# Performance work log

Measured on AMD Instinct MI355X. Metric: run time of the kernel, lower is better.

## Reference

```python
import jax, jax.numpy as jnp
import numpy as np

N = 100000

def gat_layer(x, src, dst, W, a_s, a_d, b, H, C, concat):
    # x: [N, F_in]; messages flow src -> dst, softmax grouped by dst (PyG GATConv)
    h = (x @ W).reshape(N, H, C)                       # [N,H,C]
    al_s = jnp.sum(h * a_s, axis=-1)                   # [N,H]
    al_d = jnp.sum(h * a_d, axis=-1)                   # [N,H]
    e = jax.nn.leaky_relu(al_s[src] + al_d[dst], 0.2)  # [E,H]
    m = jax.ops.segment_max(e, dst, num_segments=N)    # [N,H] per-dst max
    ex = jnp.exp(e - m[dst])
    s = jax.ops.segment_sum(ex, dst, num_segments=N)
    alpha = ex / (s[dst] + 1e-16)                      # [E,H]
    msg = h[src] * alpha[:, :, None]                   # [E,H,C]
    out = jax.ops.segment_sum(msg, dst, num_segments=N)  # [N,H,C]
    out = out.reshape(N, H * C) if concat else out.mean(axis=1)
    return out + b

def setup_inputs() -> dict:
    key = jax.random.key(0)
    ks = jax.random.split(key, 32)
    d = {}
    d['x'] = jax.random.normal(ks[0], (N, 128), dtype=jnp.float32)
    d['edge_index'] = jax.random.randint(ks[1], (2, 1600000), 0, N, dtype=jnp.int32)
    dims = [(128, 8, 8), (64, 8, 8), (64, 8, 8), (64, 8, 8), (64, 8, 40)]
    for i, (fin, H, C) in enumerate(dims, start=1):
        d[f'W{i}'] = jax.random.normal(ks[4 * i], (fin, H * C), dtype=jnp.float32) * 0.1
        d[f'as{i}'] = jax.random.normal(ks[4 * i + 1], (H, C), dtype=jnp.float32) * 0.1
        d[f'ad{i}'] = jax.random.normal(ks[4 * i + 2], (H, C), dtype=jnp.float32) * 0.1
        d[f'b{i}'] = jnp.zeros((H * C if i < 5 else C,), dtype=jnp.float32)
    return d

def reference(x, edge_index, W1, as1, ad1, b1, W2, as2, ad2, b2, W3, as3, ad3, b3, W4, as4, ad4, b4, W5, as5, ad5, b5):
    # add self-loops (PyG GATConv default add_self_loops=True)
    loop = jnp.arange(N, dtype=edge_index.dtype)
    src = jnp.concatenate([edge_index[0], loop])
    dst = jnp.concatenate([edge_index[1], loop])
    h = gat_layer(x, src, dst, W1, as1, ad1, b1, 8, 8, True)
    h = jax.nn.leaky_relu(h, 0.2)  # dropout is identity in eval mode
    h = gat_layer(h, src, dst, W2, as2, ad2, b2, 8, 8, True)
    h = jax.nn.leaky_relu(h, 0.2)
    h = gat_layer(h, src, dst, W3, as3, ad3, b3, 8, 8, True)
    h = jax.nn.leaky_relu(h, 0.2)
    h = gat_layer(h, src, dst, W4, as4, ad4, b4, 8, 8, True)
    h = jax.nn.leaky_relu(h, 0.2)
    h = gat_layer(h, src, dst, W5, as5, ad5, b5, 8, 40, False)
    return jax.nn.log_softmax(h, axis=1)
```

## Files before the change

### kernel.cpp

```cpp
#include <hip/hip_runtime.h>
#include <cstddef>
#include <cstdint>

static __device__ __forceinline__ float leaky(float x){ return x >= 0.f ? x : 0.2f*x; }
static __device__ __forceinline__ float bfl(unsigned short v){ return __uint_as_float(((unsigned)v)<<16); }
static __device__ __forceinline__ float blo(unsigned u){ return __uint_as_float(u<<16); }
static __device__ __forceinline__ float bhi(unsigned u){ return __uint_as_float(u & 0xffff0000u); }
static __device__ __forceinline__ unsigned bf16r(float f){
  unsigned u = __float_as_uint(f);
  return (u + 0x7fffu + ((u>>16)&1u)) >> 16;
}
static __device__ __forceinline__ unsigned pk(float lo, float hi){
  return bf16r(lo) | (bf16r(hi)<<16);
}

__global__ __launch_bounds__(256) void rs_hist1(const int* __restrict__ edst, int E, int N,
                                                int* __restrict__ hist, int NBLK, int Etot){
  __shared__ int lh[512];
  int t = threadIdx.x, b = blockIdx.x;
  lh[t] = 0; lh[t+256] = 0;
  __syncthreads();
  int base = b*8192;
  for (int i = 0; i < 32; i++){
    int e = base + t + i*256;
    if (e < Etot){
      int d = (e < E) ? edst[e] : (e - E);
      atomicAdd(&lh[d>>8], 1);
    }
  }
  __syncthreads();
  hist[(size_t)t*NBLK + b] = lh[t];
  hist[(size_t)(t+256)*NBLK + b] = lh[t+256];
}
__global__ __launch_bounds__(256) void s_bsum(const int* __restrict__ a, int* __restrict__ bsum, int L){
  __shared__ int sm[256];
  int t = threadIdx.x; int i = blockIdx.x*256 + t;
  sm[t] = (i < L) ? a[i] : 0;
  __syncthreads();
  #pragma unroll
  for (int o=128;o;o>>=1){ if (t<o) sm[t]+=sm[t+o]; __syncthreads(); }
  if (t==0) bsum[blockIdx.x] = sm[0];
}
__global__ __launch_bounds__(512) void k_bscan(const int* __restrict__ bsum, int* __restrict__ boff, int NB){
  __shared__ int sm[512];
  int t = threadIdx.x;
  int v = (t < NB) ? bsum[t] : 0;
  sm[t] = v; __syncthreads();
  for (int o=1;o<512;o<<=1){
    int u = (t>=o) ? sm[t-o] : 0;
    __syncthreads();
    sm[t] += u;
    __syncthreads();
  }
  if (t < NB) boff[t] = sm[t] - v;
  if (t == NB-1) boff[NB] = sm[t];
}
__global__ __launch_bounds__(256) void s_apply(const int* __restrict__ a, const int* __restrict__ boff,
                                               int* __restrict__ out, int L){
  __shared__ int sm[256];
  int t = threadIdx.x, b = blockIdx.x;
  int i = b*256 + t;
  int v = (i < L) ? a[i] : 0;
  sm[t] = v; __syncthreads();
  for (int o=1;o<256;o<<=1){
    int u = (t>=o) ? sm[t-o] : 0;
    __syncthreads();
    sm[t] += u;
    __syncthreads();
  }
  if (i < L) out[i] = boff[b] + sm[t] - v;
}
__global__ __launch_bounds__(256) void rs_scatter1(const int* __restrict__ esrc, const int* __restrict__ edst,
                                                   int E, int N, const int* __restrict__ hist2, int NBLK,
                                                   int2* __restrict__ bufA, int Etot){
  __shared__ int gb[512];
  __shared__ int lcnt[512];
  int t = threadIdx.x, b = blockIdx.x;
  gb[t]     = hist2[(size_t)t*NBLK + b];
  gb[t+256] = hist2[(size_t)(t+256)*NBLK + b];
  lcnt[t] = 0; lcnt[t+256] = 0;
  __syncthreads();
  int base = b*8192;
  for (int i = 0; i < 32; i++){
    int e = base + t + i*256;
    if (e < Etot){
      int s, d;
      if (e < E){ s = esrc[e]; d = edst[e]; }
      else { s = e - E; d = s; }
      int bin = d >> 8;
      int r = atomicAdd(&lcnt[bin], 1);
      bufA[gb[bin] + r] = make_int2(s, d);
    }
  }
}
__global__ __launch_bounds__(256) void rs_lvl2(const int2* __restrict__ bufA, const int* __restrict__ hist2,
                                               int NBLK, int* __restrict__ srcs, int* __restrict__ off,
                                               int N, int Etot){
  __shared__ int cnt[256];
  __shared__ int basev[256];
  int t = threadIdx.x, g = blockIdx.x;
  int beg = hist2[(size_t)g*NBLK];
  int end = (g < 511) ? hist2[(size_t)(g+1)*NBLK] : Etot;
  cnt[t] = 0;
  __syncthreads();
  for (int j = beg + t; j < end; j += 256)
    atomicAdd(&cnt[bufA[j].y & 255], 1);
  __syncthreads();
  int v = cnt[t];
  for (int o=1;o<256;o<<=1){
    int u = (t>=o) ? cnt[t-o] : 0;
    __syncthreads();
    cnt[t] += u;
    __syncthreads();
  }
  basev[t] = cnt[t] - v;
  __syncthreads();
  cnt[t] = 0;
  __syncthreads();
  for (int j = beg + t; j < end; j += 256){
    int2 p = bufA[j];
    int lb = p.y & 255;
    int r = atomicAdd(&cnt[lb], 1);
    srcs[beg + basev[lb] + r] = p.x;
  }
  int node = g*256 + t;
  if (node < N) off[node] = beg + basev[t];
  if (g == 0 && t == 0) off[N] = Etot;
}

template<int K, int M, bool OB>
__global__ __launch_bounds__(256) void k_gemm(
    const float* __restrict__ A, const float* __restrict__ W, int ldw, int col0,
    void* __restrict__ out, int N)
{
  constexpr int KT = 64;
  constexpr int TX = M/4;
  __shared__ float As[64][KT+1];
  __shared__ alignas(16) float Ws[KT][M];
  int t = threadIdx.x;
  int base = blockIdx.x*64;
  int tx = t % TX, ty = t / TX;
  bool act = ty < 16;
  int n0 = ty*4, m0 = tx*4;
  float acc[4][4] = {};
  for (int kt=0; kt<K; kt+=KT){
    for (int i=t; i<64*(KT/4); i+=256){
      int n  = i >> 4;
      int kq = i & 15;
      float4 v = make_float4(0.f,0.f,0.f,0.f);
      int gn = base + n;
      if (gn < N) v = *(const float4*)(A + (size_t)gn*K + kt + kq*4);
      As[n][kq*4+0]=v.x; As[n][kq*4+1]=v.y; As[n][kq*4+2]=v.z; As[n][kq*4+3]=v.w;
    }
    for (int i=t; i<KT*(M/4); i+=256){
      int k = i/(M/4), mq = i%(M/4);
      *(float4*)&Ws[k][mq*4] = *(const float4*)(W + (size_t)(kt+k)*ldw + col0 + mq*4);
    }
    __syncthreads();
    if (act){
      #pragma unroll 8
      for (int k=0;k<KT;k++){
        float4 w = *(const float4*)&Ws[k][m0];
        float av0 = As[n0+0][k], av1 = As[n0+1][k], av2 = As[n0+2][k], av3 = As[n0+3][k];
        acc[0][0]=fmaf(av0,w.x,acc[0][0]); acc[0][1]=fmaf(av0,w.y,acc[0][1]);
        acc[0][2]=fmaf(av0,w.z,acc[0][2]); acc[0][3]=fmaf(av0,w.w,acc[0][3]);
        acc[1][0]=fmaf(av1,w.x,acc[1][0]); acc[1][1]=fmaf(av1,w.y,acc[1][1]);
        acc[1][2]=fmaf(av1,w.z,acc[1][2]); acc[1][3]=fmaf(av1,w.w,acc[1][3]);
        acc[2][0]=fmaf(av2,w.x,acc[2][0]); acc[2][1]=fmaf(av2,w.y,acc[2][1]);
        acc[2][2]=fmaf(av2,w.z,acc[2][2]); acc[2][3]=fmaf(av2,w.w,acc[2][3]);
        acc[3][0]=fmaf(av3,w.x,acc[3][0]); acc[3][1]=fmaf(av3,w.y,acc[3][1]);
        acc[3][2]=fmaf(av3,w.z,acc[3][2]); acc[3][3]=fmaf(av3,w.w,acc[3][3]);
      }
    }
    __syncthreads();
  }
  if (act){
    #pragma unroll
    for (int i=0;i<4;i++){
      int gn = base + n0 + i;
      if (gn < N){
        if (OB){
          unsigned p0 = pk(acc[i][0], acc[i][1]);
          unsigned p1 = pk(acc[i][2], acc[i][3]);
          *(uint2*)((unsigned short*)out + (size_t)gn*M + m0) = make_uint2(p0, p1);
        } else {
          float4 v = make_float4(acc[i][0],acc[i][1],acc[i][2],acc[i][3]);
          *(float4*)((float*)out + (size_t)gn*M + m0) = v;
        }
      }
    }
  }
}

__global__ __launch_bounds__(320) void k_gemm5(
    const unsigned short* __restrict__ z16, const float* __restrict__ Wf,
    float* __restrict__ out5, int base, int cnt)
{
  __shared__ float As[64][65];
  __shared__ alignas(16) float Ws[64][40];
  int t = threadIdx.x;
  int rb = blockIdx.x*64;
  int tx = t % 10, ty = t / 10;
  int n0 = ty*2, m0 = tx*4;
  float acc[2][4] = {};
  for (int kt = 0; kt < 512; kt += 64){
    for (int i = t; i < 512; i += 320){
      int n = i >> 3, kq = i & 7;
      uint4 q = make_uint4(0,0,0,0);
      int ln = rb + n;
      if (ln < cnt) q = *(const uint4*)(z16 + (size_t)ln*512 + kt + kq*8);
      float* ap = &As[n][kq*8];
      ap[0]=blo(q.x); ap[1]=bhi(q.x); ap[2]=blo(q.y); ap[3]=bhi(q.y);
      ap[4]=blo(q.z); ap[5]=bhi(q.z); ap[6]=blo(q.w); ap[7]=bhi(q.w);
    }
    for (int i = t; i < 640; i += 320){
      int k = i / 10, mq = i % 10;
      *(float4*)&Ws[k][mq*4] = *(const float4*)(Wf + (size_t)(kt+k)*40 + mq*4);
    }
    __syncthreads();
    #pragma unroll 8
    for (int k=0;k<64;k++){
      float4 w = *(const float4*)&Ws[k][m0];
      float a0 = As[n0][k], a1 = As[n0+1][k];
      acc[0][0]=fmaf(a0,w.x,acc[0][0]); acc[0][1]=fmaf(a0,w.y,acc[0][1]);
      acc[0][2]=fmaf(a0,w.z,acc[0][2]); acc[0][3]=fmaf(a0,w.w,acc[0][3]);
      acc[1][0]=fmaf(a1,w.x,acc[1][0]); acc[1][1]=fmaf(a1,w.y,acc[1][1]);
      acc[1][2]=fmaf(a1,w.z,acc[1][2]); acc[1][3]=fmaf(a1,w.w,acc[1][3]);
    }
    __syncthreads();
  }
  #pragma unroll
  for (int r=0;r<2;r++){
    int ln = rb + n0 + r;
    if (ln < cnt){
      *(float4*)(out5 + (size_t)(base+ln)*40 + m0) =
        make_float4(acc[r][0],acc[r][1],acc[r][2],acc[r][3]);
    }
  }
}

__global__ void k_al(const unsigned short* __restrict__ h16, const float* __restrict__ a_s,
                     const float* __restrict__ a_d, unsigned short* __restrict__ al_s16,
                     float* __restrict__ al_d, int total )
{
  int idx = blockIdx.x*256 + threadIdx.x;
  if (idx >= total) return;
  int hd = idx & 7;
  uint4 q = *(const uint4*)(h16 + (size_t)idx*8);
  const float4* sp = (const float4*)(a_s + hd*8);
  const float4* dp = (const float4*)(a_d + hd*8);
  float4 s0 = sp[0], s1 = sp[1], d0 = dp[0], d1 = dp[1];
  float f0=blo(q.x), f1=bhi(q.x), f2=blo(q.y), f3=bhi(q.y);
  float f4=blo(q.z), f5=bhi(q.z), f6=blo(q.w), f7=bhi(q.w);
  float s = f0*s0.x + f1*s0.y + f2*s0.z + f3*s0.w
          + f4*s1.x + f5*s1.y + f6*s1.z + f7*s1.w;
  float d = f0*d0.x + f1*d0.y + f2*d0.z + f3*d0.w
          + f4*d1.x + f5*d1.y + f6*d1.z + f7*d1.w;
  al_s16[idx] = (unsigned short)bf16r(s);
  al_d[idx] = d;
}

template<bool OB>
__global__ __launch_bounds__(256) void k_agg64(
    const unsigned short* __restrict__ h16, const unsigned short* __restrict__ al16,
    const float* __restrict__ al_d, const int* __restrict__ off,
    const int* __restrict__ srcs, const float* __restrict__ bias,
    void* __restrict__ outf, int N, int apply_act)
{
  int t = threadIdx.x;
  int grp = t >> 3;
  int sub = t & 7;
  int node = blockIdx.x*32 + grp;
  if (node >= N) return;
  int beg = off[node], end = off[node+1];
  float ald = al_d[(size_t)node*8 + sub];
  float s = 0.f;
  float acc[8] = {0.f,0.f,0.f,0.f,0.f,0.f,0.f,0.f};
  int j = beg;
  for (; j+3 < end; j += 4){
    int s0 = srcs[j], s1 = srcs[j+1], s2 = srcs[j+2], s3 = srcs[j+3];
    float e0 = leaky(bfl(al16[(size_t)s0*8 + sub]) + ald);
    float e1 = leaky(bfl(al16[(size_t)s1*8 + sub]) + ald);
    float e2 = leaky(bfl(al16[(size_t)s2*8 + sub]) + ald);
    float e3 = leaky(bfl(al16[(size_t)s3*8 + sub]) + ald);
    float a0 = __expf(e0), a1 = __expf(e1), a2 = __expf(e2), a3 = __expf(e3);
    uint4 q0 = *(const uint4*)(h16 + (size_t)s0*64 + sub*8);
    uint4 q1 = *(const uint4*)(h16 + (size_t)s1*64 + sub*8);
    uint4 q2 = *(const uint4*)(h16 + (size_t)s2*64 + sub*8);
    uint4 q3 = *(const uint4*)(h16 + (size_t)s3*64 + sub*8);
    s += a0 + a1 + a2 + a3;
    acc[0]=fmaf(a0,blo(q0.x),acc[0]); acc[1]=fmaf(a0,bhi(q0.x),acc[1]);
    acc[2]=fmaf(a0,blo(q0.y),acc[2]); acc[3]=fmaf(a0,bhi(q0.y),acc[3]);
    acc[4]=fmaf(a0,blo(q0.z),acc[4]); acc[5]=fmaf(a0,bhi(q0.z),acc[5]);
    acc[6]=fmaf(a0,blo(q0.w),acc[6]); acc[7]=fmaf(a0,bhi(q0.w),acc[7]);
    acc[0]=fmaf(a1,blo(q1.x),acc[0]); acc[1]=fmaf(a1,bhi(q1.x),acc[1]);
    acc[2]=fmaf(a1,blo(q1.y),acc[2]); acc[3]=fmaf(a1,bhi(q1.y),acc[3]);
    acc[4]=fmaf(a1,blo(q1.z),acc[4]); acc[5]=fmaf(a1,bhi(q1.z),acc[5]);
    acc[6]=fmaf(a1,blo(q1.w),acc[6]); acc[7]=fmaf(a1,bhi(q1.w),acc[7]);
    acc[0]=fmaf(a2,blo(q2.x),acc[0]); acc[1]=fmaf(a2,bhi(q2.x),acc[1]);
    acc[2]=fmaf(a2,blo(q2.y),acc[2]); acc[3]=fmaf(a2,bhi(q2.y),acc[3]);
    acc[4]=fmaf(a2,blo(q2.z),acc[4]); acc[5]=fmaf(a2,bhi(q2.z),acc[5]);
    acc[6]=fmaf(a2,blo(q2.w),acc[6]); acc[7]=fmaf(a2,bhi(q2.w),acc[7]);
    acc[0]=fmaf(a3,blo(q3.x),acc[0]); acc[1]=fmaf(a3,bhi(q3.x),acc[1]);
    acc[2]=fmaf(a3,blo(q3.y),acc[2]); acc[3]=fmaf(a3,bhi(q3.y),acc[3]);
    acc[4]=fmaf(a3,blo(q3.z),acc[4]); acc[5]=fmaf(a3,bhi(q3.z),acc[5]);
    acc[6]=fmaf(a3,blo(q3.w),acc[6]); acc[7]=fmaf(a3,bhi(q3.w),acc[7]);
  }
  for (; j < end; ++j){
    int s0 = srcs[j];
    float e0 = leaky(bfl(al16[(size_t)s0*8 + sub]) + ald);
    float a0 = __expf(e0);
    uint4 q0 = *(const uint4*)(h16 + (size_t)s0*64 + sub*8);
    s += a0;
    acc[0]=fmaf(a0,blo(q0.x),acc[0]); acc[1]=fmaf(a0,bhi(q0.x),acc[1]);
    acc[2]=fmaf(a0,blo(q0.y),acc[2]); acc[3]=fmaf(a0,bhi(q0.y),acc[3]);
    acc[4]=fmaf(a0,blo(q0.z),acc[4]); acc[5]=fmaf(a0,bhi(q0.z),acc[5]);
    acc[6]=fmaf(a0,blo(q0.w),acc[6]); acc[7]=fmaf(a0,bhi(q0.w),acc[7]);
  }
  float inv = 1.f/(s + 1e-16f);
  const float4* bp = (const float4*)(bias + sub*8);
  float4 b0 = bp[0], b1 = bp[1];
  float r0 = acc[0]*inv + b0.x, r1 = acc[1]*inv + b0.y;
  float r2 = acc[2]*inv + b0.z, r3 = acc[3]*inv + b0.w;
  float r4 = acc[4]*inv + b1.x, r5 = acc[5]*inv + b1.y;
  float r6 = acc[6]*inv + b1.z, r7 = acc[7]*inv + b1.w;
  if (apply_act){
    r0=leaky(r0); r1=leaky(r1); r2=leaky(r2); r3=leaky(r3);
    r4=leaky(r4); r5=leaky(r5); r6=leaky(r6); r7=leaky(r7);
  }
  if (OB){
    uint4 o;
    o.x = pk(r0,r1); o.y = pk(r2,r3); o.z = pk(r4,r5); o.w = pk(r6,r7);
    *(uint4*)((unsigned short*)outf + (size_t)node*64 + sub*8) = o;
  } else {
    float* op = (float*)outf + (size_t)node*64 + sub*8;
    *(float4*)op = make_float4(r0,r1,r2,r3);
    *(float4*)(op+4) = make_float4(r4,r5,r6,r7);
  }
}

__global__ __launch_bounds__(512) void k_ws(const float* __restrict__ W5,
                                            const float* __restrict__ as5,
                                            const float* __restrict__ ad5,
                                            float* __restrict__ ws, float* __restrict__ wd){
  int t = threadIdx.x;
  int h = t >> 6, k = t & 63;
  float s = 0.f, d = 0.f;
  #pragma unroll 8
  for (int c=0;c<40;c++){
    float w = W5[(size_t)k*320 + h*40 + c];
    s = fmaf(w, as5[h*40+c], s);
    d = fmaf(w, ad5[h*40+c], d);
  }
  ws[h*64+k] = s; wd[h*64+k] = d;
}
__global__ void k_wf(const float* __restrict__ W5, float* __restrict__ Wf){
  int i = blockIdx.x*256 + threadIdx.x;
  if (i >= 512*40) return;
  int row = i / 40, c = i - row*40;
  int h = row >> 6, k = row & 63;
  Wf[i] = W5[(size_t)k*320 + h*40 + c];
}
__global__ void k_al5b(const unsigned short* __restrict__ f16, const float* __restrict__ ws,
                       const float* __restrict__ wd, unsigned short* __restrict__ al_s16,
                       float* __restrict__ al_d, int total )
{
  int idx = blockIdx.x*256 + threadIdx.x;
  if (idx >= total) return;
  int n = idx >> 3, h = idx & 7;
  const uint4* fp = (const uint4*)(f16 + (size_t)n*64);
  const float4* ap = (const float4*)(ws + h*64);
  const float4* bp = (const float4*)(wd + h*64);
  float s = 0.f, d = 0.f;
  #pragma unroll
  for (int q=0;q<8;q++){
    uint4 f = fp[q];
    float4 a0 = ap[q*2], a1 = ap[q*2+1];
    float4 b0 = bp[q*2], b1 = bp[q*2+1];
    float f0=blo(f.x), f1=bhi(f.x), f2=blo(f.y), f3=bhi(f.y);
    float f4=blo(f.z), f5=bhi(f.z), f6=blo(f.w), f7=bhi(f.w);
    s += f0*a0.x + f1*a0.y + f2*a0.z + f3*a0.w + f4*a1.x + f5*a1.y + f6*a1.z + f7*a1.w;
    d += f0*b0.x + f1*b0.y + f2*b0.z + f3*b0.w + f4*b1.x + f5*b1.y + f6*b1.z + f7*b1.w;
  }
  al_s16[idx] = (unsigned short)bf16r(s);
  al_d[idx] = d;
}

__global__ __launch_bounds__(256) void k_agg5z(
    const unsigned short* __restrict__ f16, const unsigned short* __restrict__ al16,
    const float* __restrict__ al_d, const int* __restrict__ off,
    const int* __restrict__ srcs, unsigned short* __restrict__ z16, int base, int cnt)
{
  int t = threadIdx.x;
  int w = t >> 6;
  int ln = blockIdx.x*4 + w;
  if (ln >= cnt) return;
  int node = base + ln;
  int tl = t & 63;
  int hd = tl & 7;
  int cb = tl >> 3;
  int beg = off[node], end = off[node+1];
  float ald = al_d[(size_t)node*8 + hd];
  int lanebase = hd*4;
  int cbo = cb*8;
  float s = 0.f;
  float acc[8] = {0.f,0.f,0.f,0.f,0.f,0.f,0.f,0.f};
  for (int jb = beg; jb < end; jb += 8){
    int j = jb + cb;
    float atil = 0.f; int si = 0;
    if (j < end){
      si = srcs[j];
      atil = __expf(leaky(bfl(al16[(size_t)si*8 + hd]) + ald));
    }
    s += atil;
    #pragma unroll 8
    for (int e = 0; e < 8; e++){
      if (jb + e >= end) break;
      float ae = __uint_as_float(__builtin_amdgcn_ds_bpermute(lanebase + e*32, __float_as_uint(atil)));
      int sie = __builtin_amdgcn_readlane(si, e*8);
      uint4 q = *(const uint4*)(f16 + (size_t)sie*64 + cbo);
      acc[0]=fmaf(ae,blo(q.x),acc[0]); acc[1]=fmaf(ae,bhi(q.x),acc[1]);
      acc[2]=fmaf(ae,blo(q.y),acc[2]); acc[3]=fmaf(ae,bhi(q.y),acc[3]);
      acc[4]=fmaf(ae,blo(q.z),acc[4]); acc[5]=fmaf(ae,bhi(q.z),acc[5]);
      acc[6]=fmaf(ae,blo(q.w),acc[6]); acc[7]=fmaf(ae,bhi(q.w),acc[7]);
    }
  }
  s += __shfl_xor(s, 8, 64);
  s += __shfl_xor(s, 16, 64);
  s += __shfl_xor(s, 32, 64);
  float inv = 1.f/(s + 1e-16f);
  uint4 o;
  o.x = pk(acc[0]*inv, acc[1]*inv);
  o.y = pk(acc[2]*inv, acc[3]*inv);
  o.z = pk(acc[4]*inv, acc[5]*inv);
  o.w = pk(acc[6]*inv, acc[7]*inv);
  *(uint4*)(z16 + (size_t)ln*512 + hd*64 + cbo) = o;
}

__global__ __launch_bounds__(256) void k_final(
    const float* __restrict__ acc, const float* __restrict__ b5,
    float* __restrict__ out, int N)
{
  int t = threadIdx.x;
  int node = blockIdx.x*4 + (t >> 6);
  if (node >= N) return;
  int tl = t & 63;
  float v = (tl < 40) ? acc[(size_t)node*40 + tl]*0.125f + b5[tl] : -1e30f;
  float m = v;
  #pragma unroll
  for (int o=32;o;o>>=1) m = fmaxf(m, __shfl_xor(m, o, 64));
  float ex = (tl < 40) ? __expf(v - m) : 0.f;
  float s = ex;
  #pragma unroll
  for (int o=32;o;o>>=1) s += __shfl_xor(s, o, 64);
  if (tl < 40) out[(size_t)node*40 + tl] = (v - m) - __logf(s);
}

extern "C" void kernel_launch(void* const* d_in, const int* in_sizes, int n_in,
                              void* d_out, int out_size, void* d_ws, size_t ws_size,
                              hipStream_t stream) {
  const float* x  = (const float*)d_in[0];
  const int*   ei = (const int*)d_in[1];
  const int N = in_sizes[0] / 128;
  const int E = in_sizes[1] / 2;
  const int* esrc = ei;
  const int* edst = ei + E;
  const float* W1 = (const float*)d_in[2];
  const float* as1= (const float*)d_in[3];
  const float* ad1= (const float*)d_in[4];
  const float* b1 = (const float*)d_in[5];
  const float* W2 = (const float*)d_in[6];
  const float* as2= (const float*)d_in[7];
  const float* ad2= (const float*)d_in[8];
  const float* b2 = (const float*)d_in[9];
  const float* W3 = (const float*)d_in[10];
  const float* as3= (const float*)d_in[11];
  const float* ad3= (const float*)d_in[12];
  const float* b3 = (const float*)d_in[13];
  const float* W4 = (const float*)d_in[14];
  const float* as4= (const float*)d_in[15];
  const float* ad4= (const float*)d_in[16];
  const float* b4 = (const float*)d_in[17];
  const float* W5 = (const float*)d_in[18];
  const float* as5= (const float*)d_in[19];
  const float* ad5= (const float*)d_in[20];
  const float* b5 = (const float*)d_in[21];

  char* p = (char*)d_ws;
  auto alloc = [&](size_t bytes)->void*{
    uintptr_t u = (uintptr_t)p;
    u = (u + 255) & ~(uintptr_t)255;
    void* r = (void*)u;
    p = (char*)u + bytes;
    return r;
  };
  const int Etot = E + N;
  const int NBLK = (Etot + 8191)/8192;
  const int L    = 512*NBLK;
  const int NB2  = (L + 255)/256;
  const int NG   = (N + 255)/256;

  int* off    = (int*)alloc((size_t)(N+1)*4);
  int* srcs   = (int*)alloc((size_t)Etot*4);
  int* hist   = (int*)alloc((size_t)L*4);
  int* hist2  = (int*)alloc((size_t)L*4);
  int* hb     = (int*)alloc((size_t)(NB2+1)*4);
  unsigned short* al_s16 = (unsigned short*)alloc((size_t)N*8*2);
  float* al_d = (float*)alloc((size_t)N*8*4);
  unsigned short* h16  = (unsigned short*)alloc((size_t)N*64*2);
  unsigned short* fB16 = (unsigned short*)alloc((size_t)N*64*2);
  float* featA= (float*)alloc((size_t)N*64*4);
  float* featB= (float*)alloc((size_t)N*64*4);
  float* wsb  = (float*)alloc((size_t)8*64*4);
  float* wdb  = (float*)alloc((size_t)8*64*4);
  float* Wf   = (float*)alloc((size_t)512*40*4);
  float* out5 = (float*)alloc((size_t)N*40*4);
  unsigned short* zbuf = (unsigned short*)featA;
  int2* bufA  = (int2*)featA;

  int gT = (N+63)/64, gA = (N+3)/4;
  int gA64 = (N+31)/32;
  int gAl = (N*8+255)/256;

  rs_hist1  <<<NBLK,256,0,stream>>>(edst, E, N, hist, NBLK, Etot);
  s_bsum    <<<NB2,256,0,stream>>>(hist, hb, L);
  k_bscan   <<<1,512,0,stream>>>(hb, hb, NB2);
  s_apply   <<<NB2,256,0,stream>>>(hist, hb, hist2, L);
  rs_scatter1<<<NBLK,256,0,stream>>>(esrc, edst, E, N, hist2, NBLK, bufA, Etot);
  rs_lvl2   <<<NG,256,0,stream>>>(bufA, hist2, NBLK, srcs, off, N, Etot);

  k_gemm<128,64,true><<<gT,256,0,stream>>>(x, W1, 64, 0, h16, N);
  k_al<<<gAl,256,0,stream>>>(h16, as1, ad1, al_s16, al_d, N*8);
  k_agg64<false><<<gA64,256,0,stream>>>(h16, al_s16, al_d, off, srcs, b1, featA, N, 1);

  k_gemm<64,64,true><<<gT,256,0,stream>>>(featA, W2, 64, 0, h16, N);
  k_al<<<gAl,256,0,stream>>>(h16, as2, ad2, al_s16, al_d, N*8);
  k_agg64<false><<<gA64,256,0,stream>>>(h16, al_s16, al_d, off, srcs, b2, featB, N, 1);

  k_gemm<64,64,true><<<gT,256,0,stream>>>(featB, W3, 64, 0, h16, N);
  k_al<<<gAl,256,0,stream>>>(h16, as3, ad3, al_s16, al_d, N*8);
  k_agg64<false><<<gA64,256,0,stream>>>(h16, al_s16, al_d, off, srcs, b3, featA, N, 1);

  k_gemm<64,64,true><<<gT,256,0,stream>>>(featA, W4, 64, 0, h16, N);
  k_al<<<gAl,256,0,stream>>>(h16, as4, ad4, al_s16, al_d, N*8);
  k_agg64<true><<<gA64,256,0,stream>>>(h16, al_s16, al_d, off, srcs, b4, fB16, N, 1);

  k_ws  <<<1,512,0,stream>>>(W5, as5, ad5, wsb, wdb);
  k_wf  <<<(512*40+255)/256,256,0,stream>>>(W5, Wf);
  k_al5b<<<gAl,256,0,stream>>>(fB16, wsb, wdb, al_s16, al_d, N*8);
  const int CH = 50000;
  for (int base = 0; base < N; base += CH){
    int cnt = (N - base < CH) ? (N - base) : CH;
    k_agg5z<<<(cnt+3)/4,256,0,stream>>>(fB16, al_s16, al_d, off, srcs, zbuf, base, cnt);
    k_gemm5<<<(cnt+63)/64,320,0,stream>>>(zbuf, Wf, out5, base, cnt);
  }

  k_final<<<gA,256,0,stream>>>(out5, b5, (float*)d_out, N);
}
```

Measured before the change: 653.3 us.

## Store intermediate features in bf16, pack sort keys, prefetch edges in final aggregation

Intermediate layer activations are written as bf16 and the GEMM gains a bf16-input load path, halving feature traffic between layers. The radix-sort scratch packs the source id and local destination bits into one 32-bit word instead of an int2. The final aggregation kernel software-prefetches the next edge batch's source and attention weight. The chunk size is halved so the scratch buffer can alias the now-dead projection buffer; this relies on N fitting in 17 bits and on buffer adjacency, and adds bf16 rounding on intermediate activations.

Result: slower. 714.7 us (+9.4%).

```diff
diff --git a/kernel.cpp b/kernel.cpp
--- a/kernel.cpp
+++ b/kernel.cpp
@@ -72,7 +72,7 @@
 }
 __global__ __launch_bounds__(256) void rs_scatter1(const int* __restrict__ esrc, const int* __restrict__ edst,
                                                    int E, int N, const int* __restrict__ hist2, int NBLK,
-                                                   int2* __restrict__ bufA, int Etot){
+                                                   int* __restrict__ bufA, int Etot){
   __shared__ int gb[512];
   __shared__ int lcnt[512];
   int t = threadIdx.x, b = blockIdx.x;
@@ -89,11 +89,11 @@
       else { s = e - E; d = s; }
       int bin = d >> 8;
       int r = atomicAdd(&lcnt[bin], 1);
-      bufA[gb[bin] + r] = make_int2(s, d);
-    }
-  }
-}
-__global__ __launch_bounds__(256) void rs_lvl2(const int2* __restrict__ bufA, const int* __restrict__ hist2,
+      bufA[gb[bin] + r] = s | ((d & 255) << 17);
+    }
+  }
+}
+__global__ __launch_bounds__(256) void rs_lvl2(const int* __restrict__ bufA, const int* __restrict__ hist2,
                                                int NBLK, int* __restrict__ srcs, int* __restrict__ off,
                                                int N, int Etot){
   __shared__ int cnt[256];
@@ -104,7 +104,7 @@
   cnt[t] = 0;
   __syncthreads();
   for (int j = beg + t; j < end; j += 256)
-    atomicAdd(&cnt[bufA[j].y & 255], 1);
+    atomicAdd(&cnt[(bufA[j] >> 17) & 255], 1);
   __syncthreads();
   int v = cnt[t];
   for (int o=1;o<256;o<<=1){
@@ -118,19 +118,19 @@
   cnt[t] = 0;
   __syncthreads();
   for (int j = beg + t; j < end; j += 256){
-    int2 p = bufA[j];
-    int lb = p.y & 255;
+    int u = bufA[j];
+    int lb = (u >> 17) & 255;
     int r = atomicAdd(&cnt[lb], 1);
-    srcs[beg + basev[lb] + r] = p.x;
+    srcs[beg + basev[lb] + r] = u & 0x1FFFF;
   }
   int node = g*256 + t;
   if (node < N) off[node] = beg + basev[t];
   if (g == 0 && t == 0) off[N] = Etot;
 }
 
-template<int K, int M, bool OB>
+template<int K, int M, bool IB, bool OB>
 __global__ __launch_bounds__(256) void k_gemm(
-    const float* __restrict__ A, const float* __restrict__ W, int ldw, int col0,
+    const void* __restrict__ Ain, const float* __restrict__ W, int ldw, int col0,
     void* __restrict__ out, int N)
 {
   constexpr int KT = 64;
@@ -144,13 +144,27 @@
   int n0 = ty*4, m0 = tx*4;
   float acc[4][4] = {};
   for (int kt=0; kt<K; kt+=KT){
-    for (int i=t; i<64*(KT/4); i+=256){
-      int n  = i >> 4;
-      int kq = i & 15;
-      float4 v = make_float4(0.f,0.f,0.f,0.f);
-      int gn = base + n;
-      if (gn < N) v = *(const float4*)(A + (size_t)gn*K + kt + kq*4);
-      As[n][kq*4+0]=v.x; As[n][kq*4+1]=v.y; As[n][kq*4+2]=v.z; As[n][kq*4+3]=v.w;
+    if (IB){
+      const unsigned short* A16 = (const unsigned short*)Ain;
+      for (int i=t; i<64*8; i+=256){
+        int n = i >> 3, kq = i & 7;
+        uint4 q = make_uint4(0,0,0,0);
+        int gn = base + n;
+        if (gn < N) q = *(const uint4*)(A16 + (size_t)gn*K + kt + kq*8);
+        float* ap = &As[n][kq*8];
+        ap[0]=blo(q.x); ap[1]=bhi(q.x); ap[2]=blo(q.y); ap[3]=bhi(q.y);
+        ap[4]=blo(q.z); ap[5]=bhi(q.z); ap[6]=blo(q.w); ap[7]=bhi(q.w);
+      }
+    } else {
+      const float* A = (const float*)Ain;
+      for (int i=t; i<64*16; i+=256){
+        int n  = i >> 4;
+        int kq = i & 15;
+        float4 v = make_float4(0.f,0.f,0.f,0.f);
+        int gn = base + n;
+        if (gn < N) v = *(const float4*)(A + (size_t)gn*K + kt + kq*4);
+        As[n][kq*4+0]=v.x; As[n][kq*4+1]=v.y; As[n][kq*4+2]=v.z; As[n][kq*4+3]=v.w;
+      }
     }
     for (int i=t; i<KT*(M/4); i+=256){
       int k = i/(M/4), mq = i%(M/4);
@@ -260,12 +274,11 @@
   al_d[idx] = d;
 }
 
-template<bool OB>
 __global__ __launch_bounds__(256) void k_agg64(
     const unsigned short* __restrict__ h16, const unsigned short* __restrict__ al16,
     const float* __restrict__ al_d, const int* __restrict__ off,
     const int* __restrict__ srcs, const float* __restrict__ bias,
-    void* __restrict__ outf, int N, int apply_act)
+    unsigned short* __restrict__ outf, int N, int apply_act)
 {
   int t = threadIdx.x;
   int grp = t >> 3;
@@ -328,15 +341,9 @@
     r0=leaky(r0); r1=leaky(r1); r2=leaky(r2); r3=leaky(r3);
     r4=leaky(r4); r5=leaky(r5); r6=leaky(r6); r7=leaky(r7);
   }
-  if (OB){
-    uint4 o;
-    o.x = pk(r0,r1); o.y = pk(r2,r3); o.z = pk(r4,r5); o.w = pk(r6,r7);
-    *(uint4*)((unsigned short*)outf + (size_t)node*64 + sub*8) = o;
-  } else {
-    float* op = (float*)outf + (size_t)node*64 + sub*8;
-    *(float4*)op = make_float4(r0,r1,r2,r3);
-    *(float4*)(op+4) = make_float4(r4,r5,r6,r7);
-  }
+  uint4 o;
+  o.x = pk(r0,r1); o.y = pk(r2,r3); o.z = pk(r4,r5); o.w = pk(r6,r7);
+  *(uint4*)(outf + (size_t)node*64 + sub*8) = o;
 }
 
 __global__ __launch_bounds__(512) void k_ws(const float* __restrict__ W5,
@@ -405,17 +412,24 @@
   int cbo = cb*8;
   float s = 0.f;
   float acc[8] = {0.f,0.f,0.f,0.f,0.f,0.f,0.f,0.f};
-  for (int jb = beg; jb < end; jb += 8){
+  int jb = beg;
+  float atil = 0.f; int si = 0;
+  {
     int j = jb + cb;
-    float atil = 0.f; int si = 0;
-    if (j < end){
-      si = srcs[j];
-      atil = __expf(leaky(bfl(al16[(size_t)si*8 + hd]) + ald));
+    if (j < end){ si = srcs[j]; atil = __expf(leaky(bfl(al16[(size_t)si*8 + hd]) + ald)); }
+  }
+  while (jb < end){
+    int jb2 = jb + 8;
+    float atil2 = 0.f; int si2 = 0;
+    {
+      int j2 = jb2 + cb;
+      if (j2 < end){ si2 = srcs[j2]; atil2 = __expf(leaky(bfl(al16[(size_t)si2*8 + hd]) + ald)); }
     }
     s += atil;
+    int nfull = end - jb; if (nfull > 8) nfull = 8;
     #pragma unroll 8
     for (int e = 0; e < 8; e++){
-      if (jb + e >= end) break;
+      if (e >= nfull) break;
       float ae = __uint_as_float(__builtin_amdgcn_ds_bpermute(lanebase + e*32, __float_as_uint(atil)));
       int sie = __builtin_amdgcn_readlane(si, e*8);
       uint4 q = *(const uint4*)(f16 + (size_t)sie*64 + cbo);
@@ -424,6 +438,7 @@
       acc[4]=fmaf(ae,blo(q.z),acc[4]); acc[5]=fmaf(ae,bhi(q.z),acc[5]);
       acc[6]=fmaf(ae,blo(q.w),acc[6]); acc[7]=fmaf(ae,bhi(q.w),acc[7]);
     }
+    atil = atil2; si = si2; jb = jb2;
   }
   s += __shfl_xor(s, 8, 64);
   s += __shfl_xor(s, 16, 64);
@@ -508,15 +523,14 @@
   unsigned short* al_s16 = (unsigned short*)alloc((size_t)N*8*2);
   float* al_d = (float*)alloc((size_t)N*8*4);
   unsigned short* h16  = (unsigned short*)alloc((size_t)N*64*2);
+  unsigned short* fA16 = (unsigned short*)alloc((size_t)N*64*2);
   unsigned short* fB16 = (unsigned short*)alloc((size_t)N*64*2);
-  float* featA= (float*)alloc((size_t)N*64*4);
-  float* featB= (float*)alloc((size_t)N*64*4);
   float* wsb  = (float*)alloc((size_t)8*64*4);
   float* wdb  = (float*)alloc((size_t)8*64*4);
   float* Wf   = (float*)alloc((size_t)512*40*4);
   float* out5 = (float*)alloc((size_t)N*40*4);
-  unsigned short* zbuf = (unsigned short*)featA;
-  int2* bufA  = (int2*)featA;
+  unsigned short* zbuf = h16;
+  int* bufA   = (int*)h16;
 
   int gT = (N+63)/64, gA = (N+3)/4;
   int gA64 = (N+31)/32;
@@ -529,26 +543,26 @@
   rs_scatter1<<<NBLK,256,0,stream>>>(esrc, edst, E, N, hist2, NBLK, bufA, Etot);
   rs_lvl2   <<<NG,256,0,stream>>>(bufA, hist2, NBLK, srcs, off, N, Etot);
 
-  k_gemm<128,64,true><<<gT,256,0,stream>>>(x, W1, 64, 0, h16, N);
+  k_gemm<128,64,false,true><<<gT,256,0,stream>>>(x, W1, 64, 0, h16, N);
   k_al<<<gAl,256,0,stream>>>(h16, as1, ad1, al_s16, al_d, N*8);
-  k_agg64<false><<<gA64,256,0,stream>>>(h16, al_s16, al_d, off, srcs, b1, featA, N, 1);
-
-  k_gemm<64,64,true><<<gT,256,0,stream>>>(featA, W2, 64, 0, h16, N);
+  k_agg64<<<gA64,256,0,stream>>>(h16, al_s16, al_d, off, srcs, b1, fA16, N, 1);
+
+  k_gemm<64,64,true,true><<<gT,256,0,stream>>>(fA16, W2, 64, 0, h16, N);
   k_al<<<gAl,256,0,stream>>>(h16, as2, ad2, al_s16, al_d, N*8);
-  k_agg64<false><<<gA64,256,0,stream>>>(h16, al_s16, al_d, off, srcs, b2, featB, N, 1);
-
-  k_gemm<64,64,true><<<gT,256,0,stream>>>(featB, W3, 64, 0, h16, N);
+  k_agg64<<<gA64,256,0,stream>>>(h16, al_s16, al_d, off, srcs, b2, fB16, N, 1);
+
+  k_gemm<64,64,true,true><<<gT,256,0,stream>>>(fB16, W3, 64, 0, h16, N);
   k_al<<<gAl,256,0,stream>>>(h16, as3, ad3, al_s16, al_d, N*8);
-  k_agg64<false><<<gA64,256,0,stream>>>(h16, al_s16, al_d, off, srcs, b3, featA, N, 1);
-
-  k_gemm<64,64,true><<<gT,256,0,stream>>>(featA, W4, 64, 0, h16, N);
+  k_agg64<<<gA64,256,0,stream>>>(h16, al_s16, al_d, off, srcs, b3, fA16, N, 1);
+
+  k_gemm<64,64,true,true><<<gT,256,0,stream>>>(fA16, W4, 64, 0, h16, N);
   k_al<<<gAl,256,0,stream>>>(h16, as4, ad4, al_s16, al_d, N*8);
-  k_agg64<true><<<gA64,256,0,stream>>>(h16, al_s16, al_d, off, srcs, b4, fB16, N, 1);
+  k_agg64<<<gA64,256,0,stream>>>(h16, al_s16, al_d, off, srcs, b4, fB16, N, 1);
 
   k_ws  <<<1,512,0,stream>>>(W5, as5, ad5, wsb, wdb);
   k_wf  <<<(512*40+255)/256,256,0,stream>>>(W5, Wf);
   k_al5b<<<gAl,256,0,stream>>>(fB16, wsb, wdb, al_s16, al_d, N*8);
-  const int CH = 50000;
+  const int CH = 25000;
   for (int base = 0; base < N; base += CH){
     int cnt = (N - base < CH) ? (N - base) : CH;
     k_agg5z<<<(cnt+3)/4,256,0,stream>>>(fB16, al_s16, al_d, off, srcs, zbuf, base, cnt);
```
